# Performance work log

Measured on AMD Instinct MI355X. Metric: run time of the kernel, lower is better.

## Reference

```python
import jax, jax.numpy as jnp
import numpy as np

NEG_SLOPE = 0.2
EPS = 1e-16


def gat_conv(x, src, dst, W, a_src, a_dst, b, num_nodes):
    # Single-head PyG GATConv (heads=1, add_self_loops already applied via src/dst).
    h = x @ W                                   # [N, C]
    alpha_s = h @ a_src                         # [N]
    alpha_d = h @ a_dst                         # [N]
    e = jax.nn.leaky_relu(alpha_s[src] + alpha_d[dst], NEG_SLOPE)  # [E]
    # softmax over incoming edges per destination node
    m = jax.ops.segment_max(e, dst, num_segments=num_nodes)        # [N]
    ex = jnp.exp(e - m[dst])
    denom = jax.ops.segment_sum(ex, dst, num_segments=num_nodes)   # [N]
    alpha = ex / (denom[dst] + EPS)                                 # [E]
    out = jax.ops.segment_sum(h[src] * alpha[:, None], dst, num_segments=num_nodes)
    return out + b


def setup_inputs() -> dict:
    key = jax.random.key(0)
    ks = jax.random.split(key, 10)
    N, E, F_in, H, C = 100000, 1600000, 64, 64, 32
    x = jax.random.normal(ks[0], (N, F_in), dtype=jnp.float32)
    edge_index = jax.random.randint(ks[1], (2, E), 0, N, dtype=jnp.int64)
    s1 = 1.0 / np.sqrt(F_in)
    s2 = 1.0 / np.sqrt(H)
    return {
        "x": x,
        "edge_index": edge_index,
        "W1": jax.random.normal(ks[2], (F_in, H), dtype=jnp.float32) * s1,
        "a1_src": jax.random.normal(ks[3], (H,), dtype=jnp.float32) * s2,
        "a1_dst": jax.random.normal(ks[4], (H,), dtype=jnp.float32) * s2,
        "b1": jnp.zeros((H,), dtype=jnp.float32),
        "W2": jax.random.normal(ks[5], (H, C), dtype=jnp.float32) * s2,
        "a2_src": jax.random.normal(ks[6], (C,), dtype=jnp.float32) / np.sqrt(C),
        "a2_dst": jax.random.normal(ks[7], (C,), dtype=jnp.float32) / np.sqrt(C),
        "b2": jnp.zeros((C,), dtype=jnp.float32),
    }


def reference(x, edge_index, W1, a1_src, a1_dst, b1, W2, a2_src, a2_dst, b2):
    N = x.shape[0]
    loops = jnp.arange(N, dtype=edge_index.dtype)
    src = jnp.concatenate([edge_index[0], loops])  # add self-loops (GATConv default)
    dst = jnp.concatenate([edge_index[1], loops])
    # dropout layers are no-ops in eval mode
    h = jax.nn.relu(gat_conv(x, src, dst, W1, a1_src, a1_dst, b1, N))
    out = gat_conv(h, src, dst, W2, a2_src, a2_dst, b2, N)
    return jax.nn.log_softmax(out, axis=-1)
```

## Files before the change

kernel.cpp:

```cpp
#include <hip/hip_runtime.h>

typedef unsigned int uint;
typedef unsigned short ushort;
typedef short short8 __attribute__((ext_vector_type(8)));
typedef float floatx4 __attribute__((ext_vector_type(4)));

#define LEAKY(e) ((e) > 0.f ? (e) : 0.2f * (e))
#define BCAP 6144
#define EPT 32
#define TILE (256 * EPT)

__device__ __forceinline__ ushort f2bf(float f) {
    uint u = __float_as_uint(f);
    return (ushort)((u + 0x7fffu + ((u >> 16) & 1u)) >> 16);
}
__device__ __forceinline__ float bflo(uint u) { return __uint_as_float(u << 16); }
__device__ __forceinline__ float bfhi(uint u) { return __uint_as_float(u & 0xffff0000u); }

__device__ __forceinline__ void binK_body(
    int bid, const int* __restrict__ srcA, const int* __restrict__ dstA,
    int* __restrict__ bcur, int* __restrict__ binned, int E, int Etot, int nbuck)
{
    __shared__ int hist[512];
    __shared__ int basep[512];
    int t = threadIdx.x;
    long long start = (long long)bid * TILE;

    hist[t] = 0; hist[t + 256] = 0;
    __syncthreads();

    short bs[EPT];
    int vals[EPT];
#pragma unroll
    for (int j = 0; j < EPT; ++j) {
        long long i = start + (long long)j * 256 + t;
        if (i < Etot) {
            int s, d;
            if (i < E) { s = srcA[i]; d = dstA[i]; } else { s = d = (int)(i - E); }
            int b = d >> 8;
            bs[j] = (short)b;
            vals[j] = (s << 8) | (d & 255);
            atomicAdd(&hist[b], 1);
        } else bs[j] = -1;
    }
    __syncthreads();

    for (int b = t; b < nbuck; b += 256) {
        int hc = hist[b];
        basep[b] = hc ? atomicAdd(bcur + b * 16, hc) : 0;
    }
    __syncthreads();
    hist[t] = 0; hist[t + 256] = 0;
    __syncthreads();

#pragma unroll
    for (int j = 0; j < EPT; ++j) {
        int b = bs[j];
        if (b >= 0) {
            int pos = basep[b] + atomicAdd(&hist[b], 1);
            if (pos < BCAP) binned[(size_t)b * BCAP + pos] = vals[j];
        }
    }
}

__device__ __forceinline__ void gemm1_body(
    int bid, const float* __restrict__ x, const float* __restrict__ W,
    const float* __restrict__ a_src, const float* __restrict__ a_dst,
    ushort* __restrict__ hb, float* __restrict__ as, float* __restrict__ ad, int N)
{
    int tid = threadIdx.x;
    int wave = tid >> 6, lane = tid & 63;
    int q = lane >> 4, c0 = lane & 15;
    int rowbase = bid * 64 + wave * 16;
    int arow = rowbase + c0;
    bool aok = arow < N;

    short8 afrag[2];
#pragma unroll
    for (int kb = 0; kb < 2; ++kb) {
        float xa[8];
        if (aok) {
            const float4 u0 = *(const float4*)(x + (size_t)arow * 64 + kb * 32 + q * 8);
            const float4 u1 = *(const float4*)(x + (size_t)arow * 64 + kb * 32 + q * 8 + 4);
            xa[0] = u0.x; xa[1] = u0.y; xa[2] = u0.z; xa[3] = u0.w;
            xa[4] = u1.x; xa[5] = u1.y; xa[6] = u1.z; xa[7] = u1.w;
        } else {
#pragma unroll
            for (int j = 0; j < 8; ++j) xa[j] = 0.f;
        }
#pragma unroll
        for (int j = 0; j < 8; ++j) afrag[kb][j] = (short)f2bf(xa[j]);
    }

    short8 bfrag[4][2];
#pragma unroll
    for (int t = 0; t < 4; ++t)
#pragma unroll
        for (int kb = 0; kb < 2; ++kb)
#pragma unroll
            for (int j = 0; j < 8; ++j)
                bfrag[t][kb][j] = (short)f2bf(W[(size_t)(kb * 32 + q * 8 + j) * 64 + t * 16 + c0]);

    floatx4 acc[4];
#pragma unroll
    for (int t = 0; t < 4; ++t) acc[t] = (floatx4){0.f, 0.f, 0.f, 0.f};
#pragma unroll
    for (int t = 0; t < 4; ++t)
#pragma unroll
        for (int kb = 0; kb < 2; ++kb)
            acc[t] = __builtin_amdgcn_mfma_f32_16x16x32_bf16(afrag[kb], bfrag[t][kb], acc[t], 0, 0, 0);

    float a_s[4], a_d[4];
#pragma unroll
    for (int t = 0; t < 4; ++t) { a_s[t] = a_src[t * 16 + c0]; a_d[t] = a_dst[t * 16 + c0]; }
    float vs[4], vd[4];
#pragma unroll
    for (int r = 0; r < 4; ++r) {
        vs[r] = 0.f; vd[r] = 0.f;
#pragma unroll
        for (int t = 0; t < 4; ++t) { vs[r] += acc[t][r] * a_s[t]; vd[r] += acc[t][r] * a_d[t]; }
    }
#pragma unroll
    for (int o = 1; o < 16; o <<= 1)
#pragma unroll
        for (int r = 0; r < 4; ++r) {
            vs[r] += __shfl_xor(vs[r], o, 16);
            vd[r] += __shfl_xor(vd[r], o, 16);
        }
    int drow = rowbase + q * 4;
    if (c0 == 0) {
#pragma unroll
        for (int r = 0; r < 4; ++r)
            if (drow + r < N) { as[drow + r] = vs[r]; ad[drow + r] = vd[r]; }
    }
#pragma unroll
    for (int r = 0; r < 4; ++r) {
        if (drow + r < N) {
#pragma unroll
            for (int t = 0; t < 4; ++t)
                hb[(size_t)(drow + r) * 64 + t * 16 + c0] = f2bf(acc[t][r]);
        }
    }
}

__global__ __launch_bounds__(256) void fusedK(
    const int* __restrict__ srcA, const int* __restrict__ dstA,
    int* __restrict__ bcur, int* __restrict__ binned, int E, int Etot, int nbuck, int tb,
    const float* __restrict__ x, const float* __restrict__ W,
    const float* __restrict__ a_src, const float* __restrict__ a_dst,
    ushort* __restrict__ hb, float* __restrict__ as, float* __restrict__ ad, int N)
{
    int b = (int)blockIdx.x;
    if (b < tb) binK_body(b, srcA, dstA, bcur, binned, E, Etot, nbuck);
    else gemm1_body(b - tb, x, W, a_src, a_dst, hb, as, ad, N);
}

__global__ __launch_bounds__(256) void bucketK(
    const int* __restrict__ bcur, const int* __restrict__ binned,
    int* __restrict__ off, int* __restrict__ csr, int N, int nbuck)
{
    __shared__ int hist[256];
    __shared__ int sh[256];
    __shared__ int cur[256];
    int b = blockIdx.x;
    int t = threadIdx.x;
    int cnt = min(bcur[b * 16], BCAP);
    const int* bin = binned + (size_t)b * BCAP;

    int partial = 0;
    for (int i = t; i < b; i += 256) partial += min(bcur[i * 16], BCAP);
    sh[t] = partial;
    __syncthreads();
#pragma unroll
    for (int o = 128; o > 0; o >>= 1) {
        if (t < o) sh[t] += sh[t + o];
        __syncthreads();
    }
    int base = sh[0];
    __syncthreads();

    hist[t] = 0;
    __syncthreads();
    for (int i = t; i < cnt; i += 256) atomicAdd(&hist[bin[i] & 255], 1);
    __syncthreads();
    int v = hist[t];
    sh[t] = v;
    __syncthreads();
#pragma unroll
    for (int o = 1; o < 256; o <<= 1) {
        int u = (t >= o) ? sh[t - o] : 0;
        __syncthreads();
        sh[t] += u;
        __syncthreads();
    }
    int excl = sh[t] - v;
    int d = b * 256 + t;
    if (d < N) off[d] = base + excl;
    if (b == nbuck - 1 && t == 0) off[N] = base + cnt;
    cur[t] = base + excl;
    __syncthreads();
    for (int i = t; i < cnt; i += 256) {
        int e = bin[i];
        int p = atomicAdd(&cur[e & 255], 1);
        csr[p] = e >> 8;
    }
}

__global__ __launch_bounds__(256) void agg1gemm2K(
    const int* __restrict__ csr_src, const int* __restrict__ off,
    const float* __restrict__ as, const float* __restrict__ ad,
    const ushort* __restrict__ hb1, const float* __restrict__ b1,
    const float* __restrict__ W,
    const float* __restrict__ a_src, const float* __restrict__ a_dst,
    ushort* __restrict__ hb2, float* __restrict__ as2, float* __restrict__ ad2, int N)
{
    __shared__ float aggL[32 * 68];
    int tid = threadIdx.x;
    int lid = tid & 7;
    int nl = tid >> 3;
    int n = blockIdx.x * 32 + nl;

    float den = 0.f;
    float acc[8];
#pragma unroll
    for (int k = 0; k < 8; ++k) acc[k] = 0.f;

    if (n < N) {
        int p0 = off[n], p1 = off[n + 1];
        float adn = ad[n];
        int base = p0;
        for (; base + 8 <= p1; base += 8) {
            int s_l = csr_src[base + lid];
            float a_l = as[s_l];
            uint4 v[8];
#pragma unroll
            for (int j = 0; j < 8; ++j) {
                int s_j = __shfl(s_l, j, 8);
                v[j] = *(const uint4*)(hb1 + (size_t)s_j * 64 + lid * 8);
            }
            float w_l = __expf(LEAKY(a_l + adn));
            den += w_l;
#pragma unroll
            for (int j = 0; j < 8; ++j) {
                float w = __shfl(w_l, j, 8);
                acc[0] += w * bflo(v[j].x); acc[1] += w * bfhi(v[j].x);
                acc[2] += w * bflo(v[j].y); acc[3] += w * bfhi(v[j].y);
                acc[4] += w * bflo(v[j].z); acc[5] += w * bfhi(v[j].z);
                acc[6] += w * bflo(v[j].w); acc[7] += w * bfhi(v[j].w);
            }
        }
        int r = p1 - base;
        if (r) {
            int s_l = 0; float w_l = 0.f;
            if (lid < r) { s_l = csr_src[base + lid]; w_l = __expf(LEAKY(as[s_l] + adn)); }
            den += w_l;
#pragma unroll
            for (int j = 0; j < 8; ++j) {
                if (j < r) {
                    int s_j = __shfl(s_l, j, 8);
                    float w = __shfl(w_l, j, 8);
                    const uint4 v = *(const uint4*)(hb1 + (size_t)s_j * 64 + lid * 8);
                    acc[0] += w * bflo(v.x); acc[1] += w * bfhi(v.x);
                    acc[2] += w * bflo(v.y); acc[3] += w * bfhi(v.y);
                    acc[4] += w * bflo(v.z); acc[5] += w * bfhi(v.z);
                    acc[6] += w * bflo(v.w); acc[7] += w * bfhi(v.w);
                }
            }
        }
#pragma unroll
        for (int o = 4; o > 0; o >>= 1) den += __shfl_xor(den, o, 8);
    } else den = 1.f;

    float inv = 1.f / den;
    float4 o0 = make_float4(acc[0] * inv, acc[1] * inv, acc[2] * inv, acc[3] * inv);
    float4 o1 = make_float4(acc[4] * inv, acc[5] * inv, acc[6] * inv, acc[7] * inv);
    *(float4*)&aggL[nl * 68 + lid * 8] = o0;
    *(float4*)&aggL[nl * 68 + lid * 8 + 4] = o1;
    __syncthreads();

    int wave = tid >> 6, lane = tid & 63;
    if (wave >= 2) return;
    int q = lane >> 4, m = lane & 15;
    int rowbase = blockIdx.x * 32 + wave * 16;

    short8 afrag[2];
#pragma unroll
    for (int kb = 0; kb < 2; ++kb) {
#pragma unroll
        for (int j = 0; j < 8; ++j) {
            float xv = aggL[(wave * 16 + m) * 68 + kb * 32 + q * 8 + j] + b1[kb * 32 + q * 8 + j];
            afrag[kb][j] = (short)f2bf(xv > 0.f ? xv : 0.f);
        }
    }

    short8 bfrag[2][2];
#pragma unroll
    for (int t = 0; t < 2; ++t)
#pragma unroll
        for (int kb = 0; kb < 2; ++kb)
#pragma unroll
            for (int j = 0; j < 8; ++j)
                bfrag[t][kb][j] = (short)f2bf(W[(size_t)(kb * 32 + q * 8 + j) * 32 + t * 16 + m]);

    floatx4 cacc[2];
#pragma unroll
    for (int t = 0; t < 2; ++t) cacc[t] = (floatx4){0.f, 0.f, 0.f, 0.f};
#pragma unroll
    for (int t = 0; t < 2; ++t)
#pragma unroll
        for (int kb = 0; kb < 2; ++kb)
            cacc[t] = __builtin_amdgcn_mfma_f32_16x16x32_bf16(afrag[kb], bfrag[t][kb], cacc[t], 0, 0, 0);

    float a_s[2], a_d[2];
#pragma unroll
    for (int t = 0; t < 2; ++t) { a_s[t] = a_src[t * 16 + m]; a_d[t] = a_dst[t * 16 + m]; }
    float vs[4], vd[4];
#pragma unroll
    for (int r = 0; r < 4; ++r) {
        vs[r] = 0.f; vd[r] = 0.f;
#pragma unroll
        for (int t = 0; t < 2; ++t) { vs[r] += cacc[t][r] * a_s[t]; vd[r] += cacc[t][r] * a_d[t]; }
    }
#pragma unroll
    for (int o = 1; o < 16; o <<= 1)
#pragma unroll
        for (int r = 0; r < 4; ++r) {
            vs[r] += __shfl_xor(vs[r], o, 16);
            vd[r] += __shfl_xor(vd[r], o, 16);
        }
    int drow = rowbase + q * 4;
    if (m == 0) {
#pragma unroll
        for (int r = 0; r < 4; ++r)
            if (drow + r < N) { as2[drow + r] = vs[r]; ad2[drow + r] = vd[r]; }
    }
#pragma unroll
    for (int r = 0; r < 4; ++r) {
        if (drow + r < N) {
#pragma unroll
            for (int t = 0; t < 2; ++t)
                hb2[(size_t)(drow + r) * 32 + t * 16 + m] = f2bf(cacc[t][r]);
        }
    }
}

__global__ __launch_bounds__(256) void node_agg2(
    const int* __restrict__ csr_src, const int* __restrict__ off,
    const float* __restrict__ as, const float* __restrict__ ad,
    const ushort* __restrict__ hb, const float* __restrict__ b2,
    float* __restrict__ out, int N)
{
    int tid = threadIdx.x;
    int lid = tid & 3;
    int n = blockIdx.x * 64 + (tid >> 2);
    if (n >= N) return;
    int p0 = off[n], p1 = off[n + 1];
    float adn = ad[n];

    float den = 0.f;
    float acc[8];
#pragma unroll
    for (int k = 0; k < 8; ++k) acc[k] = 0.f;

    int base = p0;
    for (; base + 4 <= p1; base += 4) {
        int s_l = csr_src[base + lid];
        float a_l = as[s_l];
        uint4 v[4];
#pragma unroll
        for (int j = 0; j < 4; ++j) {
            int s_j = __shfl(s_l, j, 4);
            v[j] = *(const uint4*)(hb + (size_t)s_j * 32 + lid * 8);
        }
        float w_l = __expf(LEAKY(a_l + adn));
        den += w_l;
#pragma unroll
        for (int j = 0; j < 4; ++j) {
            float w = __shfl(w_l, j, 4);
            acc[0] += w * bflo(v[j].x); acc[1] += w * bfhi(v[j].x);
            acc[2] += w * bflo(v[j].y); acc[3] += w * bfhi(v[j].y);
            acc[4] += w * bflo(v[j].z); acc[5] += w * bfhi(v[j].z);
            acc[6] += w * bflo(v[j].w); acc[7] += w * bfhi(v[j].w);
        }
    }
    int r = p1 - base;
    if (r) {
        int s_l = 0; float w_l = 0.f;
        if (lid < r) { s_l = csr_src[base + lid]; w_l = __expf(LEAKY(as[s_l] + adn)); }
        den += w_l;
#pragma unroll
        for (int j = 0; j < 4; ++j) {
            if (j < r) {
                int s_j = __shfl(s_l, j, 4);
                float w = __shfl(w_l, j, 4);
                const uint4 v = *(const uint4*)(hb + (size_t)s_j * 32 + lid * 8);
                acc[0] += w * bflo(v.x); acc[1] += w * bfhi(v.x);
                acc[2] += w * bflo(v.y); acc[3] += w * bfhi(v.y);
                acc[4] += w * bflo(v.z); acc[5] += w * bfhi(v.z);
                acc[6] += w * bflo(v.w); acc[7] += w * bfhi(v.w);
            }
        }
    }
#pragma unroll
    for (int o = 2; o > 0; o >>= 1) den += __shfl_xor(den, o, 4);
    float inv = 1.f / den;
#pragma unroll
    for (int k = 0; k < 8; ++k) acc[k] = acc[k] * inv + b2[lid * 8 + k];

    float mx = acc[0];
#pragma unroll
    for (int k = 1; k < 8; ++k) mx = fmaxf(mx, acc[k]);
#pragma unroll
    for (int o = 2; o > 0; o >>= 1) mx = fmaxf(mx, __shfl_xor(mx, o, 4));
    float se = 0.f;
#pragma unroll
    for (int k = 0; k < 8; ++k) se += __expf(acc[k] - mx);
#pragma unroll
    for (int o = 2; o > 0; o >>= 1) se += __shfl_xor(se, o, 4);
    float lse = mx + __logf(se);
    float4 o0 = make_float4(acc[0] - lse, acc[1] - lse, acc[2] - lse, acc[3] - lse);
    float4 o1 = make_float4(acc[4] - lse, acc[5] - lse, acc[6] - lse, acc[7] - lse);
    float* op = out + (size_t)n * 32 + lid * 8;
    *(float4*)op = o0;
    *(float4*)(op + 4) = o1;
}

extern "C" void kernel_launch(void* const* d_in, const int* in_sizes, int n_in,
                              void* d_out, int out_size, void* d_ws, size_t ws_size,
                              hipStream_t stream) {
    const float* x   = (const float*)d_in[0];
    const int*   ei  = (const int*)d_in[1];
    const float* W1  = (const float*)d_in[2];
    const float* a1s = (const float*)d_in[3];
    const float* a1d = (const float*)d_in[4];
    const float* b1  = (const float*)d_in[5];
    const float* W2  = (const float*)d_in[6];
    const float* a2s = (const float*)d_in[7];
    const float* a2d = (const float*)d_in[8];
    const float* b2  = (const float*)d_in[9];

    int N = in_sizes[0] / 64;
    int E = in_sizes[1] / 2;
    int Etot = E + N;
    int nbuck = (N + 255) >> 8;
    const int* srcA = ei;
    const int* dstA = ei + E;

    float* ws = (float*)d_ws;
    ushort* hb1 = (ushort*)ws;
    ushort* hb2 = hb1 + (size_t)N * 64;
    float* as1  = ws + (size_t)N * 48;
    float* ad1  = as1 + N;
    float* as2  = ad1 + N;
    float* ad2  = as2 + N;
    int* off    = (int*)(ad2 + N);
    int* bcur   = off + (N + 1);
    int* csr    = bcur + (size_t)nbuck * 16;
    int* binned = csr + Etot;

    hipMemsetAsync(bcur, 0, sizeof(int) * (size_t)nbuck * 16, stream);

    int tb = (int)(((long long)Etot + TILE - 1) / TILE);
    int g1 = (N + 63) / 64;

    fusedK<<<tb + g1, 256, 0, stream>>>(srcA, dstA, bcur, binned, E, Etot, nbuck, tb,
                                        x, W1, a1s, a1d, hb1, as1, ad1, N);
    bucketK<<<nbuck, 256, 0, stream>>>(bcur, binned, off, csr, N, nbuck);
    agg1gemm2K<<<(N + 31) / 32, 256, 0, stream>>>(csr, off, as1, ad1, hb1, b1, W2,
                                                  a2s, a2d, hb2, as2, ad2, N);
    node_agg2<<<(N + 63) / 64, 256, 0, stream>>>(csr, off, as2, ad2, hb2, b2,
                                                 (float*)d_out, N);
}
```

Baseline: 209.1 us.

## Fuse bucket CSR build into layer-1 aggregation using 64-node buckets in shared memory

Buckets are narrowed from 256 to 64 destination nodes, and the separate bucket-to-CSR kernel is folded into the layer-1 aggregation plus GEMM2 kernel, now launched with 512 threads. Each block builds its local CSR in shared memory and reads neighbours from it directly, while still writing a padded global CSR with per-node offsets and degrees for layer 2. This removes one launch, the cross-bucket prefix sum, and a global round trip of the CSR. In exchange the binning histogram in shared memory grows to 2048 entries, and a bucket holding more than 1536 edges would silently drop edges.

Result: faster. 204.0 us (-2.5%).

```diff
diff --git a/kernel.cpp b/kernel.cpp
--- a/kernel.cpp
+++ b/kernel.cpp
@@ -6,7 +6,8 @@
 typedef float floatx4 __attribute__((ext_vector_type(4)));
 
 #define LEAKY(e) ((e) > 0.f ? (e) : 0.2f * (e))
-#define BCAP 6144
+#define BCAP 1536
+#define NBMAX 2048
 #define EPT 32
 #define TILE (256 * EPT)
 
@@ -21,12 +22,12 @@
     int bid, const int* __restrict__ srcA, const int* __restrict__ dstA,
     int* __restrict__ bcur, int* __restrict__ binned, int E, int Etot, int nbuck)
 {
-    __shared__ int hist[512];
-    __shared__ int basep[512];
+    __shared__ int hist[NBMAX];
+    __shared__ int basep[NBMAX];
     int t = threadIdx.x;
     long long start = (long long)bid * TILE;
 
-    hist[t] = 0; hist[t + 256] = 0;
+    for (int i = t; i < NBMAX; i += 256) hist[i] = 0;
     __syncthreads();
 
     short bs[EPT];
@@ -37,9 +38,9 @@
         if (i < Etot) {
             int s, d;
             if (i < E) { s = srcA[i]; d = dstA[i]; } else { s = d = (int)(i - E); }
-            int b = d >> 8;
+            int b = d >> 6;
             bs[j] = (short)b;
-            vals[j] = (s << 8) | (d & 255);
+            vals[j] = (s << 6) | (d & 63);
             atomicAdd(&hist[b], 1);
         } else bs[j] = -1;
     }
@@ -50,7 +51,7 @@
         basep[b] = hc ? atomicAdd(bcur + b * 16, hc) : 0;
     }
     __syncthreads();
-    hist[t] = 0; hist[t + 256] = 0;
+    for (int i = t; i < NBMAX; i += 256) hist[i] = 0;
     __syncthreads();
 
 #pragma unroll
@@ -155,70 +156,56 @@
     else gemm1_body(b - tb, x, W, a_src, a_dst, hb, as, ad, N);
 }
 
-__global__ __launch_bounds__(256) void bucketK(
+__global__ __launch_bounds__(512) void bagg1gemm2K(
     const int* __restrict__ bcur, const int* __restrict__ binned,
-    int* __restrict__ off, int* __restrict__ csr, int N, int nbuck)
-{
-    __shared__ int hist[256];
-    __shared__ int sh[256];
-    __shared__ int cur[256];
-    int b = blockIdx.x;
-    int t = threadIdx.x;
-    int cnt = min(bcur[b * 16], BCAP);
-    const int* bin = binned + (size_t)b * BCAP;
-
-    int partial = 0;
-    for (int i = t; i < b; i += 256) partial += min(bcur[i * 16], BCAP);
-    sh[t] = partial;
-    __syncthreads();
-#pragma unroll
-    for (int o = 128; o > 0; o >>= 1) {
-        if (t < o) sh[t] += sh[t + o];
-        __syncthreads();
-    }
-    int base = sh[0];
-    __syncthreads();
-
-    hist[t] = 0;
-    __syncthreads();
-    for (int i = t; i < cnt; i += 256) atomicAdd(&hist[bin[i] & 255], 1);
-    __syncthreads();
-    int v = hist[t];
-    sh[t] = v;
-    __syncthreads();
-#pragma unroll
-    for (int o = 1; o < 256; o <<= 1) {
-        int u = (t >= o) ? sh[t - o] : 0;
-        __syncthreads();
-        sh[t] += u;
-        __syncthreads();
-    }
-    int excl = sh[t] - v;
-    int d = b * 256 + t;
-    if (d < N) off[d] = base + excl;
-    if (b == nbuck - 1 && t == 0) off[N] = base + cnt;
-    cur[t] = base + excl;
-    __syncthreads();
-    for (int i = t; i < cnt; i += 256) {
-        int e = bin[i];
-        int p = atomicAdd(&cur[e & 255], 1);
-        csr[p] = e >> 8;
-    }
-}
-
-__global__ __launch_bounds__(256) void agg1gemm2K(
-    const int* __restrict__ csr_src, const int* __restrict__ off,
+    int* __restrict__ csr, int* __restrict__ off, int* __restrict__ deg_out,
     const float* __restrict__ as, const float* __restrict__ ad,
     const ushort* __restrict__ hb1, const float* __restrict__ b1,
     const float* __restrict__ W,
     const float* __restrict__ a_src, const float* __restrict__ a_dst,
     ushort* __restrict__ hb2, float* __restrict__ as2, float* __restrict__ ad2, int N)
 {
-    __shared__ float aggL[32 * 68];
-    int tid = threadIdx.x;
-    int lid = tid & 7;
-    int nl = tid >> 3;
-    int n = blockIdx.x * 32 + nl;
+    __shared__ int histL[64];
+    __shared__ int offL[64];
+    __shared__ int curL[64];
+    __shared__ int csrL[BCAP];
+    __shared__ float aggL[64 * 68];
+    int b = blockIdx.x;
+    int t = threadIdx.x;
+    int cnt = min(bcur[b * 16], BCAP);
+    const int* bin = binned + (size_t)b * BCAP;
+
+    if (t < 64) histL[t] = 0;
+    __syncthreads();
+    for (int i = t; i < cnt; i += 512) atomicAdd(&histL[bin[i] & 63], 1);
+    __syncthreads();
+    if (t < 64) {
+        int v = histL[t];
+        int x = v;
+#pragma unroll
+        for (int o = 1; o < 64; o <<= 1) {
+            int y = __shfl_up(x, o, 64);
+            if (t >= o) x += y;
+        }
+        int excl = x - v;
+        offL[t] = excl;
+        curL[t] = excl;
+        int d = b * 64 + t;
+        if (d < N) { off[d] = b * BCAP + excl; deg_out[d] = v; }
+    }
+    __syncthreads();
+    for (int i = t; i < cnt; i += 512) {
+        int e = bin[i];
+        int p = atomicAdd(&curL[e & 63], 1);
+        int s = e >> 6;
+        csrL[p] = s;
+        csr[(size_t)b * BCAP + p] = s;
+    }
+    __syncthreads();
+
+    int lid = t & 7;
+    int nl = t >> 3;
+    int n = b * 64 + nl;
 
     float den = 0.f;
     float acc[8];
@@ -226,11 +213,12 @@
     for (int k = 0; k < 8; ++k) acc[k] = 0.f;
 
     if (n < N) {
-        int p0 = off[n], p1 = off[n + 1];
+        int p0 = offL[nl];
+        int pend = p0 + histL[nl];
         float adn = ad[n];
         int base = p0;
-        for (; base + 8 <= p1; base += 8) {
-            int s_l = csr_src[base + lid];
+        for (; base + 8 <= pend; base += 8) {
+            int s_l = csrL[base + lid];
             float a_l = as[s_l];
             uint4 v[8];
 #pragma unroll
@@ -249,10 +237,10 @@
                 acc[6] += w * bflo(v[j].w); acc[7] += w * bfhi(v[j].w);
             }
         }
-        int r = p1 - base;
+        int r = pend - base;
         if (r) {
             int s_l = 0; float w_l = 0.f;
-            if (lid < r) { s_l = csr_src[base + lid]; w_l = __expf(LEAKY(as[s_l] + adn)); }
+            if (lid < r) { s_l = csrL[base + lid]; w_l = __expf(LEAKY(as[s_l] + adn)); }
             den += w_l;
 #pragma unroll
             for (int j = 0; j < 8; ++j) {
@@ -278,10 +266,10 @@
     *(float4*)&aggL[nl * 68 + lid * 8 + 4] = o1;
     __syncthreads();
 
-    int wave = tid >> 6, lane = tid & 63;
-    if (wave >= 2) return;
+    int wave = t >> 6, lane = t & 63;
+    if (wave >= 4) return;
     int q = lane >> 4, m = lane & 15;
-    int rowbase = blockIdx.x * 32 + wave * 16;
+    int rowbase = b * 64 + wave * 16;
 
     short8 afrag[2];
 #pragma unroll
@@ -295,31 +283,31 @@
 
     short8 bfrag[2][2];
 #pragma unroll
-    for (int t = 0; t < 2; ++t)
+    for (int tt = 0; tt < 2; ++tt)
 #pragma unroll
         for (int kb = 0; kb < 2; ++kb)
 #pragma unroll
             for (int j = 0; j < 8; ++j)
-                bfrag[t][kb][j] = (short)f2bf(W[(size_t)(kb * 32 + q * 8 + j) * 32 + t * 16 + m]);
+                bfrag[tt][kb][j] = (short)f2bf(W[(size_t)(kb * 32 + q * 8 + j) * 32 + tt * 16 + m]);
 
     floatx4 cacc[2];
 #pragma unroll
-    for (int t = 0; t < 2; ++t) cacc[t] = (floatx4){0.f, 0.f, 0.f, 0.f};
-#pragma unroll
-    for (int t = 0; t < 2; ++t)
+    for (int tt = 0; tt < 2; ++tt) cacc[tt] = (floatx4){0.f, 0.f, 0.f, 0.f};
+#pragma unroll
+    for (int tt = 0; tt < 2; ++tt)
 #pragma unroll
         for (int kb = 0; kb < 2; ++kb)
-            cacc[t] = __builtin_amdgcn_mfma_f32_16x16x32_bf16(afrag[kb], bfrag[t][kb], cacc[t], 0, 0, 0);
+            cacc[tt] = __builtin_amdgcn_mfma_f32_16x16x32_bf16(afrag[kb], bfrag[tt][kb], cacc[tt], 0, 0, 0);
 
     float a_s[2], a_d[2];
 #pragma unroll
-    for (int t = 0; t < 2; ++t) { a_s[t] = a_src[t * 16 + m]; a_d[t] = a_dst[t * 16 + m]; }
+    for (int tt = 0; tt < 2; ++tt) { a_s[tt] = a_src[tt * 16 + m]; a_d[tt] = a_dst[tt * 16 + m]; }
     float vs[4], vd[4];
 #pragma unroll
     for (int r = 0; r < 4; ++r) {
         vs[r] = 0.f; vd[r] = 0.f;
 #pragma unroll
-        for (int t = 0; t < 2; ++t) { vs[r] += cacc[t][r] * a_s[t]; vd[r] += cacc[t][r] * a_d[t]; }
+        for (int tt = 0; tt < 2; ++tt) { vs[r] += cacc[tt][r] * a_s[tt]; vd[r] += cacc[tt][r] * a_d[tt]; }
     }
 #pragma unroll
     for (int o = 1; o < 16; o <<= 1)
@@ -338,14 +326,15 @@
     for (int r = 0; r < 4; ++r) {
         if (drow + r < N) {
 #pragma unroll
-            for (int t = 0; t < 2; ++t)
-                hb2[(size_t)(drow + r) * 32 + t * 16 + m] = f2bf(cacc[t][r]);
+            for (int tt = 0; tt < 2; ++tt)
+                hb2[(size_t)(drow + r) * 32 + tt * 16 + m] = f2bf(cacc[tt][r]);
         }
     }
 }
 
 __global__ __launch_bounds__(256) void node_agg2(
     const int* __restrict__ csr_src, const int* __restrict__ off,
+    const int* __restrict__ deg,
     const float* __restrict__ as, const float* __restrict__ ad,
     const ushort* __restrict__ hb, const float* __restrict__ b2,
     float* __restrict__ out, int N)
@@ -354,7 +343,7 @@
     int lid = tid & 3;
     int n = blockIdx.x * 64 + (tid >> 2);
     if (n >= N) return;
-    int p0 = off[n], p1 = off[n + 1];
+    int p0 = off[n], p1 = p0 + deg[n];
     float adn = ad[n];
 
     float den = 0.f;
@@ -442,7 +431,7 @@
     int N = in_sizes[0] / 64;
     int E = in_sizes[1] / 2;
     int Etot = E + N;
-    int nbuck = (N + 255) >> 8;
+    int nbuck = (N + 63) >> 6;
     const int* srcA = ei;
     const int* dstA = ei + E;
 
@@ -454,9 +443,10 @@
     float* as2  = ad1 + N;
     float* ad2  = as2 + N;
     int* off    = (int*)(ad2 + N);
-    int* bcur   = off + (N + 1);
+    int* deg    = off + N;
+    int* bcur   = deg + N;
     int* csr    = bcur + (size_t)nbuck * 16;
-    int* binned = csr + Etot;
+    int* binned = csr + (size_t)nbuck * BCAP;
 
     hipMemsetAsync(bcur, 0, sizeof(int) * (size_t)nbuck * 16, stream);
 
@@ -465,9 +455,9 @@
 
     fusedK<<<tb + g1, 256, 0, stream>>>(srcA, dstA, bcur, binned, E, Etot, nbuck, tb,
                                         x, W1, a1s, a1d, hb1, as1, ad1, N);
-    bucketK<<<nbuck, 256, 0, stream>>>(bcur, binned, off, csr, N, nbuck);
-    agg1gemm2K<<<(N + 31) / 32, 256, 0, stream>>>(csr, off, as1, ad1, hb1, b1, W2,
-                                                  a2s, a2d, hb2, as2, ad2, N);
-    node_agg2<<<(N + 63) / 64, 256, 0, stream>>>(csr, off, as2, ad2, hb2, b2,
+    bagg1gemm2K<<<nbuck, 512, 0, stream>>>(bcur, binned, csr, off, deg,
+                                           as1, ad1, hb1, b1, W2, a2s, a2d,
+                                           hb2, as2, ad2, N);
+    node_agg2<<<(N + 63) / 64, 256, 0, stream>>>(csr, off, deg, as2, ad2, hb2, b2,
                                                  (float*)d_out, N);
 }
```
